# Optimization experiments

Hardware: AMD Instinct MI355X
Metric: run time of the kernel (lower is better)

The kernel has to match this reference:

```python
import jax, jax.numpy as jnp
import numpy as np


def setup_inputs() -> dict:
    key = jax.random.key(0)
    k1, k2, k3 = jax.random.split(key, 3)
    B, H, W = 4, 1080, 1920
    Sh, Sw, Sl = 16, 16, 8
    pixels = jax.random.uniform(k1, (B, H, W, 3), dtype=jnp.float32)
    coords = jax.random.uniform(k2, (B, H, W, 2), dtype=jnp.float32)
    # identity affine grid + small perturbation (learned parameter)
    identity = jnp.zeros((Sh, Sw, Sl, 12), dtype=jnp.float32)
    identity = identity.at[..., 0].set(1.0).at[..., 5].set(1.0).at[..., 10].set(1.0)
    grid = identity + 0.1 * jax.random.normal(k3, (Sh, Sw, Sl, 12), dtype=jnp.float32)
    return {"pixels": pixels, "coords": coords, "grid": grid}


def _bilateral_apply(pixels, coords, grid):
    orig_shape = pixels.shape[:-1]
    p = pixels.reshape(-1, 3)        # (N, 3)
    c = coords.reshape(-1, 2)        # (N, 2)
    Sh, Sw, Sl = grid.shape[0], grid.shape[1], grid.shape[2]

    # guide = luminance
    guide = 0.2126 * p[:, 0] + 0.7152 * p[:, 1] + 0.0722 * p[:, 2]

    gx = jnp.clip(c[:, 0] * (Sw - 1), 0.0, Sw - 1.001)
    gy = jnp.clip(c[:, 1] * (Sh - 1), 0.0, Sh - 1.001)
    gz = jnp.clip(jnp.clip(guide, 0.0, 1.0) * (Sl - 1), 0.0, Sl - 1.001)

    y0 = jnp.floor(gy).astype(jnp.int32)
    x0 = jnp.floor(gx).astype(jnp.int32)
    z0 = jnp.floor(gz).astype(jnp.int32)
    y1 = jnp.minimum(y0 + 1, Sh - 1)
    x1 = jnp.minimum(x0 + 1, Sw - 1)
    z1 = jnp.minimum(z0 + 1, Sl - 1)

    fy = (gy - y0.astype(gy.dtype))[:, None]
    fx = (gx - x0.astype(gx.dtype))[:, None]
    fz = (gz - z0.astype(gz.dtype))[:, None]

    c000 = grid[y0, x0, z0]
    c001 = grid[y0, x0, z1]
    c010 = grid[y0, x1, z0]
    c011 = grid[y0, x1, z1]
    c100 = grid[y1, x0, z0]
    c101 = grid[y1, x0, z1]
    c110 = grid[y1, x1, z0]
    c111 = grid[y1, x1, z1]

    c00 = c000 + (c001 - c000) * fz
    c01 = c010 + (c011 - c010) * fz
    c10 = c100 + (c101 - c100) * fz
    c11 = c110 + (c111 - c110) * fz
    c0 = c00 + (c01 - c00) * fx
    c1 = c10 + (c11 - c10) * fx
    coeffs = c0 + (c1 - c0) * fy      # (N, 12)

    A = coeffs.reshape(-1, 3, 4)
    # affine: A[:, :, :3] @ rgb + A[:, :, 3]  (equivalent to cat with ones)
    out = jnp.einsum('nij,nj->ni', A[:, :, :3], p) + A[:, :, 3]
    return out.reshape(*orig_shape, 3)


def reference(pixels, coords, grid):
    return _bilateral_apply(pixels, coords, grid)
```

## Files before the change

kernel.cpp:

```cpp
#include <hip/hip_runtime.h>


typedef _Float16 h4 __attribute__((ext_vector_type(4)));
typedef _Float16 h8 __attribute__((ext_vector_type(8)));

#define BLOCK 1024

#define XSA 72
#define YSA 1152
#define NA  18432
#define XSB 56
#define YSB 896
#define NB  14336

__global__ __launch_bounds__(BLOCK) void bilateral_apply(
    const float* __restrict__ pixels,
    const float* __restrict__ coords,
    const float* __restrict__ grid,
    float* __restrict__ out,
    int n4)
{
    __shared__ alignas(16) _Float16 gA[NA];
    __shared__ alignas(16) _Float16 gB[NB];

    const int stride = gridDim.x * BLOCK;
    int t = blockIdx.x * BLOCK + threadIdx.x;

    long long base = (long long)t * 4;
    const float* pp = pixels + base * 3;
    const float* cp = coords + base * 2;
    float4 pa = *(const float4*)(pp + 0);
    float4 pb = *(const float4*)(pp + 4);
    float4 pc = *(const float4*)(pp + 8);
    float4 ca = *(const float4*)(cp + 0);
    float4 cb = *(const float4*)(cp + 4);

    for (int cell = threadIdx.x; cell < 2048; cell += BLOCK) {
        int y = cell >> 7;
        int x = (cell >> 3) & 15;
        int z = cell & 7;
        const float4* src = (const float4*)(grid + (long long)cell * 12);
        float4 v0 = src[0], v1 = src[1], v2 = src[2];
        h8 a = { (_Float16)v0.x, (_Float16)v0.y, (_Float16)v0.z, (_Float16)v0.w,
                 (_Float16)v1.x, (_Float16)v1.y, (_Float16)v1.z, (_Float16)v1.w };
        *(h8*)(gA + y * YSA + x * XSA + z * 8) = a;
        h4 b = { (_Float16)v2.x, (_Float16)v2.y, (_Float16)v2.z, (_Float16)v2.w };
        _Float16* bb = gB + y * YSB + x * XSB;
        if (z <= 6) *(h4*)(bb + z * 8) = b;
        if (z >= 1) *(h4*)(bb + (z - 1) * 8 + 4) = b;
    }
    __syncthreads();

    #pragma clang loop unroll(disable)
    while (true) {
        int tn = t + stride;
        bool more = tn < n4;
        float4 npa, npb, npc, nca, ncb;
        if (more) {
            long long nbase = (long long)tn * 4;
            const float* npp = pixels + nbase * 3;
            const float* ncp = coords + nbase * 2;
            npa = *(const float4*)(npp + 0);
            npb = *(const float4*)(npp + 4);
            npc = *(const float4*)(npp + 8);
            nca = *(const float4*)(ncp + 0);
            ncb = *(const float4*)(ncp + 4);
        }
        __builtin_amdgcn_sched_barrier(0);

        float R[4]  = {pa.x, pa.w, pb.z, pc.y};
        float G[4]  = {pa.y, pb.x, pb.w, pc.z};
        float Bc[4] = {pa.z, pb.y, pc.x, pc.w};
        float CX[4] = {ca.x, ca.z, cb.x, cb.z};
        float CY[4] = {ca.y, ca.w, cb.y, cb.w};

        float O[12];

        #pragma unroll
        for (int k = 0; k < 4; ++k) {
            float r = R[k], g = G[k], b = Bc[k];
            float guide = 0.2126f * r + 0.7152f * g + 0.0722f * b;

            float gx = fminf(fmaxf(CX[k] * 15.0f, 0.0f), 14.999f);
            float gy = fminf(fmaxf(CY[k] * 15.0f, 0.0f), 14.999f);
            float gz = fminf(fminf(fmaxf(guide, 0.0f), 1.0f) * 7.0f, 6.999f);

            int x0 = (int)gx, y0 = (int)gy, z0 = (int)gz;
            float fx = gx - (float)x0;
            float fy = gy - (float)y0;
            float fz = gz - (float)z0;

            int abase = y0 * YSA + x0 * XSA + z0 * 8;
            int bbase = y0 * YSB + x0 * XSB + z0 * 8;
            const int aoff[4] = {0, XSA, YSA, YSA + XSA};
            const int boff[4] = {0, XSB, YSB, YSB + XSB};
            float wz0 = 1.0f - fz, wz1 = fz;
            float cw[4] = {(1.0f - fy) * (1.0f - fx), (1.0f - fy) * fx,
                           fy * (1.0f - fx),           fy * fx};

            h8 accA = (h8)(_Float16)0.0f;
            h4 accB = (h4)(_Float16)0.0f;

            #pragma unroll
            for (int c = 0; c < 4; ++c) {
                const h8* qa = (const h8*)(gA + abase + aoff[c]);
                h8 alo = qa[0];
                h8 ahi = qa[1];
                h8 qb  = *(const h8*)(gB + bbase + boff[c]);
                _Float16 u0 = (_Float16)(cw[c] * wz0);
                _Float16 u1 = (_Float16)(cw[c] * wz1);
                h8 u0v8 = {u0, u0, u0, u0, u0, u0, u0, u0};
                h8 u1v8 = {u1, u1, u1, u1, u1, u1, u1, u1};
                accA = alo * u0v8 + (ahi * u1v8 + accA);
                h4 blo = __builtin_shufflevector(qb, qb, 0, 1, 2, 3);
                h4 bhi = __builtin_shufflevector(qb, qb, 4, 5, 6, 7);
                h4 u0v4 = {u0, u0, u0, u0};
                h4 u1v4 = {u1, u1, u1, u1};
                accB = blo * u0v4 + (bhi * u1v4 + accB);
            }

            h4 acc0 = __builtin_shufflevector(accA, accA, 0, 1, 2, 3);
            h4 acc1 = __builtin_shufflevector(accA, accA, 4, 5, 6, 7);

            O[3 * k + 0] = fmaf((float)acc0.x, r, fmaf((float)acc0.y, g,
                           fmaf((float)acc0.z, b, (float)acc0.w)));
            O[3 * k + 1] = fmaf((float)acc1.x, r, fmaf((float)acc1.y, g,
                           fmaf((float)acc1.z, b, (float)acc1.w)));
            O[3 * k + 2] = fmaf((float)accB.x, r, fmaf((float)accB.y, g,
                           fmaf((float)accB.z, b, (float)accB.w)));
        }

        float* op = out + base * 3;
        *(float4*)(op + 0) = make_float4(O[0], O[1], O[2],  O[3]);
        *(float4*)(op + 4) = make_float4(O[4], O[5], O[6],  O[7]);
        *(float4*)(op + 8) = make_float4(O[8], O[9], O[10], O[11]);

        if (!more) break;
        pa = npa; pb = npb; pc = npc; ca = nca; cb = ncb;
        t = tn;
        base = (long long)t * 4;
    }
}

extern "C" void kernel_launch(void* const* d_in, const int* in_sizes, int n_in,
                              void* d_out, int out_size, void* d_ws, size_t ws_size,
                              hipStream_t stream) {
    const float* pixels = (const float*)d_in[0];
    const float* coords = (const float*)d_in[1];
    const float* grid   = (const float*)d_in[2];
    float* out = (float*)d_out;

    int npix = in_sizes[0] / 3;
    int n4   = npix / 4;
    int nblk = 512;
    bilateral_apply<<<nblk, BLOCK, 0, stream>>>(pixels, coords, grid, out, n4);
}
```

Before: 230.9 us.

## Move third coefficient row from LDS to a global fp16 table

Drops the gB shared-memory table, which holds the third output row's coefficients. Those coefficients now come from a z-pair-packed fp16 table built in workspace by a small prep kernel and are read through the global/L1 path, with a fallback that reads the raw grid. The aim is to shrink LDS use and cut the block's setup staging. In exchange it adds a second kernel launch and per-pixel global gathers, and it replaces the vectorized float4 output stores with scalar stores.

```diff
diff --git a/kernel.cpp b/kernel.cpp
--- a/kernel.cpp
+++ b/kernel.cpp
@@ -1,6 +1,7 @@
 #include <hip/hip_runtime.h>
 
 
+typedef _Float16 h2 __attribute__((ext_vector_type(2)));
 typedef _Float16 h4 __attribute__((ext_vector_type(4)));
 typedef _Float16 h8 __attribute__((ext_vector_type(8)));
 
@@ -9,19 +10,32 @@
 #define XSA 72
 #define YSA 1152
 #define NA  18432
-#define XSB 56
-#define YSB 896
-#define NB  14336
 
+#define BT_BYTES 28672
+
+__global__ void prep_b(const float* __restrict__ grid,
+                       _Float16* __restrict__ bt) {
+    int zp = blockIdx.x;
+    int c  = threadIdx.x;
+    const float4* gr = (const float4*)grid;
+    int cell8 = c * 8;
+    float4 lo = gr[(cell8 + zp) * 3 + 2];
+    float4 hi = gr[(cell8 + zp + 1) * 3 + 2];
+    h8 v = { (_Float16)lo.x, (_Float16)lo.y, (_Float16)lo.z, (_Float16)lo.w,
+             (_Float16)hi.x, (_Float16)hi.y, (_Float16)hi.z, (_Float16)hi.w };
+    *(h8*)(bt + (c * 7 + zp) * 8) = v;
+}
+
+template <bool WS>
 __global__ __launch_bounds__(BLOCK) void bilateral_apply(
     const float* __restrict__ pixels,
     const float* __restrict__ coords,
     const float* __restrict__ grid,
+    const _Float16* __restrict__ bt,
     float* __restrict__ out,
     int n4)
 {
     __shared__ alignas(16) _Float16 gA[NA];
-    __shared__ alignas(16) _Float16 gB[NB];
 
     const int stride = gridDim.x * BLOCK;
     int t = blockIdx.x * BLOCK + threadIdx.x;
@@ -40,14 +54,10 @@
         int x = (cell >> 3) & 15;
         int z = cell & 7;
         const float4* src = (const float4*)(grid + (long long)cell * 12);
-        float4 v0 = src[0], v1 = src[1], v2 = src[2];
+        float4 v0 = src[0], v1 = src[1];
         h8 a = { (_Float16)v0.x, (_Float16)v0.y, (_Float16)v0.z, (_Float16)v0.w,
                  (_Float16)v1.x, (_Float16)v1.y, (_Float16)v1.z, (_Float16)v1.w };
         *(h8*)(gA + y * YSA + x * XSA + z * 8) = a;
-        h4 b = { (_Float16)v2.x, (_Float16)v2.y, (_Float16)v2.z, (_Float16)v2.w };
-        _Float16* bb = gB + y * YSB + x * XSB;
-        if (z <= 6) *(h4*)(bb + z * 8) = b;
-        if (z >= 1) *(h4*)(bb + (z - 1) * 8 + 4) = b;
     }
     __syncthreads();
 
@@ -74,8 +84,6 @@
         float CX[4] = {ca.x, ca.z, cb.x, cb.z};
         float CY[4] = {ca.y, ca.w, cb.y, cb.w};
 
-        float O[12];
-
         #pragma unroll
         for (int k = 0; k < 4; ++k) {
             float r = R[k], g = G[k], b = Bc[k];
@@ -91,29 +99,54 @@
             float fz = gz - (float)z0;
 
             int abase = y0 * YSA + x0 * XSA + z0 * 8;
-            int bbase = y0 * YSB + x0 * XSB + z0 * 8;
-            const int aoff[4] = {0, XSA, YSA, YSA + XSA};
-            const int boff[4] = {0, XSB, YSB, YSB + XSB};
+
+            h8 qb[4];
+            if constexpr (WS) {
+                const h8* bq = (const h8*)bt + ((y0 * 16 + x0) * 7 + z0);
+                qb[0] = bq[0];
+                qb[1] = bq[7];
+                qb[2] = bq[112];
+                qb[3] = bq[119];
+            } else {
+                const float4* gr = (const float4*)grid;
+                int c8 = (y0 * 16 + x0) * 8 + z0;
+                const int co[4] = {0, 8 * 8, 16 * 8 * 8, 17 * 8 * 8};
+                #pragma unroll
+                for (int c = 0; c < 4; ++c) {
+                    int cc = c8 + ((c & 1) ? 8 : 0) + ((c & 2) ? 128 : 0);
+                    float4 lo = gr[cc * 3 + 2];
+                    float4 hi = gr[(cc + 1) * 3 + 2];
+                    qb[c] = h8{ (_Float16)lo.x, (_Float16)lo.y, (_Float16)lo.z, (_Float16)lo.w,
+                                (_Float16)hi.x, (_Float16)hi.y, (_Float16)hi.z, (_Float16)hi.w };
+                }
+                (void)co;
+            }
+
             float wz0 = 1.0f - fz, wz1 = fz;
-            float cw[4] = {(1.0f - fy) * (1.0f - fx), (1.0f - fy) * fx,
-                           fy * (1.0f - fx),           fy * fx};
+            float cw0 = (1.0f - fy) * (1.0f - fx);
+            float cw1 = (1.0f - fy) * fx;
+            float cw2 = fy * (1.0f - fx);
+            float cw3 = fy * fx;
+            h2 w[4] = { h2{(_Float16)(cw0 * wz0), (_Float16)(cw0 * wz1)},
+                        h2{(_Float16)(cw1 * wz0), (_Float16)(cw1 * wz1)},
+                        h2{(_Float16)(cw2 * wz0), (_Float16)(cw2 * wz1)},
+                        h2{(_Float16)(cw3 * wz0), (_Float16)(cw3 * wz1)} };
 
+            const int ao[4] = {0, XSA, YSA, YSA + XSA};
             h8 accA = (h8)(_Float16)0.0f;
             h4 accB = (h4)(_Float16)0.0f;
 
             #pragma unroll
             for (int c = 0; c < 4; ++c) {
-                const h8* qa = (const h8*)(gA + abase + aoff[c]);
-                h8 alo = qa[0];
-                h8 ahi = qa[1];
-                h8 qb  = *(const h8*)(gB + bbase + boff[c]);
-                _Float16 u0 = (_Float16)(cw[c] * wz0);
-                _Float16 u1 = (_Float16)(cw[c] * wz1);
+                const h8* qa = (const h8*)(gA + abase + ao[c]);
+                h8 a0 = qa[0];
+                h8 a1 = qa[1];
+                _Float16 u0 = w[c].x, u1 = w[c].y;
                 h8 u0v8 = {u0, u0, u0, u0, u0, u0, u0, u0};
                 h8 u1v8 = {u1, u1, u1, u1, u1, u1, u1, u1};
-                accA = alo * u0v8 + (ahi * u1v8 + accA);
-                h4 blo = __builtin_shufflevector(qb, qb, 0, 1, 2, 3);
-                h4 bhi = __builtin_shufflevector(qb, qb, 4, 5, 6, 7);
+                accA = a0 * u0v8 + (a1 * u1v8 + accA);
+                h4 blo = __builtin_shufflevector(qb[c], qb[c], 0, 1, 2, 3);
+                h4 bhi = __builtin_shufflevector(qb[c], qb[c], 4, 5, 6, 7);
                 h4 u0v4 = {u0, u0, u0, u0};
                 h4 u1v4 = {u1, u1, u1, u1};
                 accB = blo * u0v4 + (bhi * u1v4 + accB);
@@ -121,19 +154,15 @@
 
             h4 acc0 = __builtin_shufflevector(accA, accA, 0, 1, 2, 3);
             h4 acc1 = __builtin_shufflevector(accA, accA, 4, 5, 6, 7);
-
-            O[3 * k + 0] = fmaf((float)acc0.x, r, fmaf((float)acc0.y, g,
-                           fmaf((float)acc0.z, b, (float)acc0.w)));
-            O[3 * k + 1] = fmaf((float)acc1.x, r, fmaf((float)acc1.y, g,
-                           fmaf((float)acc1.z, b, (float)acc1.w)));
-            O[3 * k + 2] = fmaf((float)accB.x, r, fmaf((float)accB.y, g,
-                           fmaf((float)accB.z, b, (float)accB.w)));
+            float o0 = fmaf((float)acc0.x, r, fmaf((float)acc0.y, g,
+                       fmaf((float)acc0.z, b, (float)acc0.w)));
+            float o1 = fmaf((float)acc1.x, r, fmaf((float)acc1.y, g,
+                       fmaf((float)acc1.z, b, (float)acc1.w)));
+            float o2 = fmaf((float)accB.x, r, fmaf((float)accB.y, g,
+                       fmaf((float)accB.z, b, (float)accB.w)));
+            float* op = out + (base + k) * 3;
+            op[0] = o0; op[1] = o1; op[2] = o2;
         }
-
-        float* op = out + base * 3;
-        *(float4*)(op + 0) = make_float4(O[0], O[1], O[2],  O[3]);
-        *(float4*)(op + 4) = make_float4(O[4], O[5], O[6],  O[7]);
-        *(float4*)(op + 8) = make_float4(O[8], O[9], O[10], O[11]);
 
         if (!more) break;
         pa = npa; pb = npb; pc = npc; ca = nca; cb = ncb;
@@ -153,5 +182,14 @@
     int npix = in_sizes[0] / 3;
     int n4   = npix / 4;
     int nblk = 512;
-    bilateral_apply<<<nblk, BLOCK, 0, stream>>>(pixels, coords, grid, out, n4);
+
+    if (d_ws != nullptr && ws_size >= BT_BYTES) {
+        _Float16* bt = (_Float16*)d_ws;
+        prep_b<<<7, 256, 0, stream>>>(grid, bt);
+        bilateral_apply<true><<<nblk, BLOCK, 0, stream>>>(
+            pixels, coords, grid, bt, out, n4);
+    } else {
+        bilateral_apply<false><<<nblk, BLOCK, 0, stream>>>(
+            pixels, coords, grid, nullptr, out, n4);
+    }
 }
```

Result: slower. 272.6 us (+18.1%).
